# Performance work log

Hardware: AMD Instinct MI355X
Metric: run time of the kernel (lower is better)

## Reference

```python
import jax, jax.numpy as jnp
import numpy as np

B, L, E, H = 1024, 50, 256, 256
NEG = -1e9          # stands in for -inf masked_fill (exp(NEG) == 0 in fp32)
C_EXPL = 10.0       # tanh_exploration for the pointer head
N_GLIMPSES = 1


def setup_inputs() -> dict:
    key = jax.random.key(0)
    ks = jax.random.split(key, 20)
    s = 1.0 / np.sqrt(H).astype(np.float32)
    return {
        "decoder_input": jax.random.normal(ks[0], (B, E), jnp.float32),
        "embedded_inputs": jax.random.normal(ks[1], (L, B, E), jnp.float32),
        "h0": jax.random.normal(ks[2], (B, H), jnp.float32),
        "c0": jax.random.normal(ks[3], (B, H), jnp.float32),
        "context": jax.random.normal(ks[4], (L, B, H), jnp.float32),
        "init_mask": jnp.zeros((B, L), dtype=bool),
        "lstm_Wih": jax.random.normal(ks[5], (4 * H, E), jnp.float32) * s,
        "lstm_Whh": jax.random.normal(ks[6], (4 * H, H), jnp.float32) * s,
        "lstm_bih": jax.random.normal(ks[7], (4 * H,), jnp.float32) * s,
        "lstm_bhh": jax.random.normal(ks[8], (4 * H,), jnp.float32) * s,
        "gl_Wq": jax.random.normal(ks[9], (H, H), jnp.float32) * s,
        "gl_bq": jax.random.normal(ks[10], (H,), jnp.float32) * s,
        "gl_Wref": jax.random.normal(ks[11], (H, H), jnp.float32) * s,
        "gl_bref": jax.random.normal(ks[12], (H,), jnp.float32) * s,
        "gl_v": jax.random.uniform(ks[13], (H,), jnp.float32, -s, s),
        "pt_Wq": jax.random.normal(ks[14], (H, H), jnp.float32) * s,
        "pt_bq": jax.random.normal(ks[15], (H, H // H * H,)[:1] and (H,), jnp.float32) * s,
        "pt_Wref": jax.random.normal(ks[16], (H, H), jnp.float32) * s,
        "pt_bref": jax.random.normal(ks[17], (H,), jnp.float32) * s,
        "pt_v": jax.random.uniform(ks[18], (H,), jnp.float32, -s, s),
    }


def _attention(Wq, bq, Wref, bref, v, query, context, use_tanh):
    # context: [L,B,H], query: [B,H]
    e = jnp.einsum('lbh,oh->lbo', context, Wref) + bref      # conv1d(k=1) proj of ref
    q = query @ Wq.T + bq                                    # [B,H]
    u = jnp.einsum('lbh,h->bl', jnp.tanh(q[None, :, :] + e), v)
    if use_tanh:
        u = C_EXPL * jnp.tanh(u)
    return e, u


def _lstm_cell(x, h, c, Wih, Whh, bih, bhh):
    g = x @ Wih.T + bih + h @ Whh.T + bhh
    i, f, gg, o = jnp.split(g, 4, axis=1)   # torch LSTMCell gate order: i,f,g,o
    c2 = jax.nn.sigmoid(f) * c + jax.nn.sigmoid(i) * jnp.tanh(gg)
    h2 = jax.nn.sigmoid(o) * jnp.tanh(c2)
    return h2, c2


def reference(decoder_input, embedded_inputs, h0, c0, context, init_mask,
              lstm_Wih, lstm_Whh, lstm_bih, lstm_bhh,
              gl_Wq, gl_bq, gl_Wref, gl_bref, gl_v,
              pt_Wq, pt_bq, pt_Wref, pt_bref, pt_v):
    batch_idx = jnp.arange(B)

    def step(carry, t):
        h, c, mask, idxs, dec_in = carry
        # update_mask(mask, selected), skipped at step 0 (prev_idxs is None)
        safe = jnp.maximum(idxs, 0)
        m2 = mask.at[batch_idx, safe].set(True)
        m2 = m2.at[:, -1].set(jnp.where(m2.all(axis=1), False, m2[:, -1]))
        logit_mask = jnp.where(t == 0, mask, m2)
        # LSTM cell
        hy, cy = _lstm_cell(dec_in, h, c, lstm_Wih, lstm_Whh, lstm_bih, lstm_bhh)
        g_l = hy
        # glimpse attention(s) (mask_glimpses=True)
        for _ in range(N_GLIMPSES):
            e, gl = _attention(gl_Wq, gl_bq, gl_Wref, gl_bref, gl_v, g_l, context, False)
            gl = jnp.where(logit_mask, NEG, gl)
            g_l = jnp.einsum('lbh,bl->bh', e, jax.nn.softmax(gl, axis=1))
        # pointer attention (mask_logits=True)
        _, logits = _attention(pt_Wq, pt_bq, pt_Wref, pt_bref, pt_v, g_l, context, True)
        logits = jnp.where(logit_mask, NEG, logits)
        log_p = jax.nn.log_softmax(logits, axis=1)          # [B,L]
        new_idxs = jax.lax.stop_gradient(jnp.argmax(log_p, axis=1))  # greedy decode (detached)
        new_dec_in = embedded_inputs[new_idxs, batch_idx]   # gather next input [B,E]
        return (hy, cy, logit_mask, new_idxs, new_dec_in), (log_p, new_idxs)

    init = (h0, c0, init_mask, jnp.full((B,), -1, dtype=jnp.int32), decoder_input)
    _, (log_ps, sels) = jax.lax.scan(step, init, jnp.arange(L))
    # stack along time dim 1, as torch.stack(outputs, 1)
    return jnp.transpose(log_ps, (1, 0, 2)), jnp.transpose(sels, (1, 0))
```

## Files before the change

kernel.cpp:

```cpp
#include <hip/hip_runtime.h>
#include <math.h>

#define Bsz 1024
#define Lsz 50
#define Esz 256
#define Hsz 256
#define NEGV (-1e9f)

__global__ void init_kernel(const float* __restrict__ dec0,
                            float* __restrict__ dec,
                            int* __restrict__ mask)
{
    int i = blockIdx.x * 256 + threadIdx.x;
    dec[i] = dec0[i];
    if (i < Bsz * Lsz) mask[i] = 0;
}

__global__ void transpose_wq(const float* __restrict__ WqGl, const float* __restrict__ WqPt,
                             float* __restrict__ WqGlT, float* __restrict__ WqPtT)
{
    int k = blockIdx.x;
    int n = threadIdx.x;
    if (blockIdx.y == 0) WqGlT[k * 256 + n] = WqGl[n * 256 + k];
    else                 WqPtT[k * 256 + n] = WqPt[n * 256 + k];
}

__global__ __launch_bounds__(256) void eproj_kernel(const float* __restrict__ A,
                                                    const float* __restrict__ W,
                                                    const float* __restrict__ bias,
                                                    float* __restrict__ Eo)
{
    __shared__ __align__(16) float As[16][68];
    __shared__ __align__(16) float Bs[16][68];
    const int tid = threadIdx.x;
    const int tx = tid & 15, ty = tid >> 4;
    const int ml = tid >> 2;
    const int kb = (tid & 3) << 2;

    const int x = blockIdx.x;
    const int xcd = x & 7;
    const int j = x >> 3;
    const int mt = xcd * 100 + (j >> 2);
    const int nt = j & 3;
    const int m0 = mt * 64, n0 = nt * 64;

    const int K = Hsz;
    float acc[4][4] = {};
    for (int k0 = 0; k0 < K; k0 += 16) {
        float4 a4 = *(const float4*)(A + (size_t)(m0 + ml) * K + k0 + kb);
        float4 b4 = *(const float4*)(W + (size_t)(n0 + ml) * K + k0 + kb);
        As[kb+0][ml] = a4.x; As[kb+1][ml] = a4.y; As[kb+2][ml] = a4.z; As[kb+3][ml] = a4.w;
        Bs[kb+0][ml] = b4.x; Bs[kb+1][ml] = b4.y; Bs[kb+2][ml] = b4.z; Bs[kb+3][ml] = b4.w;
        __syncthreads();
#pragma unroll
        for (int kk = 0; kk < 16; kk++) {
            float4 av = *(const float4*)(&As[kk][ty << 2]);
            float4 bv = *(const float4*)(&Bs[kk][tx << 2]);
            float a_[4] = {av.x, av.y, av.z, av.w};
            float b_[4] = {bv.x, bv.y, bv.z, bv.w};
#pragma unroll
            for (int i = 0; i < 4; i++)
#pragma unroll
                for (int j2 = 0; j2 < 4; j2++) acc[i][j2] = fmaf(a_[i], b_[j2], acc[i][j2]);
        }
        __syncthreads();
    }
#pragma unroll
    for (int i = 0; i < 4; i++) {
        int m = m0 + (ty << 2) + i;
        int bb = m & (Bsz - 1);
        int ll = m >> 10;
#pragma unroll
        for (int j2 = 0; j2 < 4; j2++) {
            int n = n0 + (tx << 2) + j2;
            Eo[(size_t)bb * Lsz * Hsz + (size_t)ll * Hsz + n] = acc[i][j2] + bias[n];
        }
    }
}

__global__ __launch_bounds__(256) void lstm_fused(
    const float* __restrict__ dec, const float* __restrict__ hprev,
    const float* __restrict__ cin,
    const float* __restrict__ Wih, const float* __restrict__ Whh,
    const float* __restrict__ bih, const float* __restrict__ bhh,
    float* __restrict__ hout, float* __restrict__ cout)
{
    __shared__ __align__(16) float As[16][68];
    __shared__ __align__(16) float Bs[16][68];
    const int tid = threadIdx.x;
    const int tx = tid & 15, ty = tid >> 4;
    const int ml = tid >> 2;
    const int kb = (tid & 3) << 2;
    const int m0 = blockIdx.x * 64;
    const int hh0 = blockIdx.y * 16;
    const int wrow = ((ml >> 4) << 8) + hh0 + (ml & 15);
    const int pcol = ((ml & 15) << 2) + (ml >> 4);

    float4 a4 = *(const float4*)(dec + (size_t)(m0 + ml) * 256 + kb);
    float4 b4 = *(const float4*)(Wih + (size_t)wrow * 256 + kb);

    float acc[4][4] = {};
    for (int k0 = 0; k0 < 512; k0 += 16) {
        As[kb+0][ml] = a4.x; As[kb+1][ml] = a4.y; As[kb+2][ml] = a4.z; As[kb+3][ml] = a4.w;
        Bs[kb+0][pcol] = b4.x; Bs[kb+1][pcol] = b4.y; Bs[kb+2][pcol] = b4.z; Bs[kb+3][pcol] = b4.w;
        __syncthreads();
        int k1 = k0 + 16;
        if (k1 < 512) {
            const float* A = (k1 < 256) ? dec : hprev;
            const float* W = (k1 < 256) ? Wih : Whh;
            int kk0 = k1 & 255;
            a4 = *(const float4*)(A + (size_t)(m0 + ml) * 256 + kk0 + kb);
            b4 = *(const float4*)(W + (size_t)wrow * 256 + kk0 + kb);
        }
#pragma unroll
        for (int kk = 0; kk < 16; kk++) {
            float4 av = *(const float4*)(&As[kk][ty << 2]);
            float4 bv = *(const float4*)(&Bs[kk][tx << 2]);
            float a_[4] = {av.x, av.y, av.z, av.w};
            float b_[4] = {bv.x, bv.y, bv.z, bv.w};
#pragma unroll
            for (int i = 0; i < 4; i++)
#pragma unroll
                for (int j = 0; j < 4; j++) acc[i][j] = fmaf(a_[i], b_[j], acc[i][j]);
        }
        __syncthreads();
    }

    const int hh = hh0 + tx;
    const float bi0 = bih[hh]       + bhh[hh];
    const float bf  = bih[256 + hh] + bhh[256 + hh];
    const float bg  = bih[512 + hh] + bhh[512 + hh];
    const float bo  = bih[768 + hh] + bhh[768 + hh];
#pragma unroll
    for (int i = 0; i < 4; i++) {
        int m = m0 + (ty << 2) + i;
        float gi = acc[i][0] + bi0;
        float gf = acc[i][1] + bf;
        float gc = acc[i][2] + bg;
        float go = acc[i][3] + bo;
        float ii = 1.0f / (1.0f + expf(-gi));
        float ff = 1.0f / (1.0f + expf(-gf));
        float oo = 1.0f / (1.0f + expf(-go));
        float c2 = ff * cin[(size_t)m * 256 + hh] + ii * tanhf(gc);
        hout[(size_t)m * 256 + hh] = oo * tanhf(c2);
        cout[(size_t)m * 256 + hh] = c2;
    }
}

__global__ __launch_bounds__(256) void attn_row(
    const float* __restrict__ h,
    const float* __restrict__ WqGlT, const float* __restrict__ glbq,
    const float* __restrict__ e_gl, const float* __restrict__ glv,
    const float* __restrict__ WqPtT, const float* __restrict__ ptbq,
    const float* __restrict__ e_pt, const float* __restrict__ ptv,
    int* __restrict__ mask, float* __restrict__ out, int t,
    float* __restrict__ dec, const float* __restrict__ emb)
{
    __shared__ float h_s[256];
    __shared__ __align__(16) float q_s[256];
    __shared__ float g_s[256];
    __shared__ float u_s[64];
    __shared__ float p_s[64];
    __shared__ int sel_s;

    const int tid = threadIdx.x;
    const int lane = tid & 63, wave = tid >> 6;
    const int b = blockIdx.x;

    h_s[tid] = h[(size_t)b * 256 + tid];
    __syncthreads();

    float q = glbq[tid];
#pragma unroll 8
    for (int k = 0; k < 256; k++)
        q = fmaf(h_s[k], WqGlT[(size_t)k * 256 + tid], q);
    q_s[tid] = q;
    __syncthreads();

    const float* ebg = e_gl + (size_t)b * Lsz * 256;
    {
        const float4 q4 = ((const float4*)q_s)[lane];
        const float4 v4 = ((const float4*)glv)[lane];
#pragma unroll
        for (int lp = 0; lp < 13; lp++) {
            const int l = lp * 4 + wave;
            float x = 0.0f;
            if (l < Lsz) {
                float4 e4 = *(const float4*)(ebg + (size_t)l * 256 + (lane << 2));
                x  = v4.x * tanhf(q4.x + e4.x);
                x += v4.y * tanhf(q4.y + e4.y);
                x += v4.z * tanhf(q4.z + e4.z);
                x += v4.w * tanhf(q4.w + e4.w);
            }
#pragma unroll
            for (int o = 32; o > 0; o >>= 1) x += __shfl_xor(x, o, 64);
            if (lane == 0 && l < Lsz) u_s[l] = x;
        }
    }
    __syncthreads();

    if (wave == 0) {
        const int l = lane;
        const int ml = (l < Lsz) ? mask[b * Lsz + l] : 0;
        float logit = (l < Lsz) ? (ml ? NEGV : u_s[l]) : -1e30f;
        float m = logit;
#pragma unroll
        for (int o = 32; o > 0; o >>= 1) m = fmaxf(m, __shfl_xor(m, o, 64));
        float ex = (l < Lsz) ? expf(logit - m) : 0.0f;
        float den = ex;
#pragma unroll
        for (int o = 32; o > 0; o >>= 1) den += __shfl_xor(den, o, 64);
        if (l < Lsz) p_s[l] = ex / den;
    }
    __syncthreads();

    {
        float acc = 0.0f;
        const float* ebh = ebg + tid;
#pragma unroll
        for (int l = 0; l < Lsz; l++)
            acc = fmaf(p_s[l], ebh[(size_t)l * 256], acc);
        g_s[tid] = acc;
    }
    __syncthreads();

    float p = ptbq[tid];
#pragma unroll 8
    for (int k = 0; k < 256; k++)
        p = fmaf(g_s[k], WqPtT[(size_t)k * 256 + tid], p);
    q_s[tid] = p;
    __syncthreads();

    const float* ebp = e_pt + (size_t)b * Lsz * 256;
    {
        const float4 q4 = ((const float4*)q_s)[lane];
        const float4 v4 = ((const float4*)ptv)[lane];
#pragma unroll
        for (int lp = 0; lp < 13; lp++) {
            const int l = lp * 4 + wave;
            float x = 0.0f;
            if (l < Lsz) {
                float4 e4 = *(const float4*)(ebp + (size_t)l * 256 + (lane << 2));
                x  = v4.x * tanhf(q4.x + e4.x);
                x += v4.y * tanhf(q4.y + e4.y);
                x += v4.z * tanhf(q4.z + e4.z);
                x += v4.w * tanhf(q4.w + e4.w);
            }
#pragma unroll
            for (int o = 32; o > 0; o >>= 1) x += __shfl_xor(x, o, 64);
            if (lane == 0 && l < Lsz) u_s[l] = x;
        }
    }
    __syncthreads();

    if (wave == 0) {
        const int l = lane;
        const int ml = (l < Lsz) ? mask[b * Lsz + l] : 0;
        float logit;
        if (l < Lsz) {
            float u = u_s[l];
            logit = 10.0f * tanhf(u);
            if (ml) logit = NEGV;
        } else logit = -1e30f;

        float m = logit;
#pragma unroll
        for (int o = 32; o > 0; o >>= 1) m = fmaxf(m, __shfl_xor(m, o, 64));
        float ex = (l < Lsz) ? expf(logit - m) : 0.0f;
        float den = ex;
#pragma unroll
        for (int o = 32; o > 0; o >>= 1) den += __shfl_xor(den, o, 64);

        float av = logit; int ai = (l < Lsz) ? l : 63;
#pragma unroll
        for (int o = 32; o > 0; o >>= 1) {
            float ov = __shfl_xor(av, o, 64);
            int   oi = __shfl_xor(ai, o, 64);
            if (ov > av || (ov == av && oi < ai)) { av = ov; ai = oi; }
        }
        const float lse = m + logf(den);
        if (l < Lsz)
            out[(size_t)b * Lsz * Lsz + (size_t)t * Lsz + l] = logit - lse;
        if (l == 0) {
            out[(size_t)Bsz * Lsz * Lsz + (size_t)b * Lsz + t] = (float)ai;
            sel_s = ai;
        }
        int newm = ml | (l == ai);
        unsigned long long bal = __ballot(l >= Lsz ? 1 : newm);
        int all = (bal == 0xFFFFFFFFFFFFFFFFull);
        if (l < Lsz) mask[b * Lsz + l] = (all && l == Lsz - 1) ? 0 : newm;
    }
    __syncthreads();

    {
        const int s = sel_s;
        dec[(size_t)b * 256 + tid] = emb[(size_t)s * Bsz * 256 + (size_t)b * 256 + tid];
    }
}

extern "C" void kernel_launch(void* const* d_in, const int* in_sizes, int n_in,
                              void* d_out, int out_size, void* d_ws, size_t ws_size,
                              hipStream_t stream) {
    const float* decoder_input = (const float*)d_in[0];
    const float* emb           = (const float*)d_in[1];
    const float* h0            = (const float*)d_in[2];
    const float* c0            = (const float*)d_in[3];
    const float* context       = (const float*)d_in[4];
    const float* Wih    = (const float*)d_in[6];
    const float* Whh    = (const float*)d_in[7];
    const float* bih    = (const float*)d_in[8];
    const float* bhh    = (const float*)d_in[9];
    const float* glWq   = (const float*)d_in[10];
    const float* glbq   = (const float*)d_in[11];
    const float* glWref = (const float*)d_in[12];
    const float* glbref = (const float*)d_in[13];
    const float* glv    = (const float*)d_in[14];
    const float* ptWq   = (const float*)d_in[15];
    const float* ptbq   = (const float*)d_in[16];
    const float* ptWref = (const float*)d_in[17];
    const float* ptbref = (const float*)d_in[18];
    const float* ptv    = (const float*)d_in[19];

    float* out = (float*)d_out;

    float* ws    = (float*)d_ws;
    float* e_gl  = ws;
    float* e_pt  = e_gl + (size_t)Bsz * Lsz * Hsz;
    float* WqGlT = e_pt + (size_t)Bsz * Lsz * Hsz;
    float* WqPtT = WqGlT + (size_t)Hsz * Hsz;
    float* hb0   = WqPtT + (size_t)Hsz * Hsz;
    float* hb1   = hb0 + (size_t)Bsz * Hsz;
    float* cb0   = hb1 + (size_t)Bsz * Hsz;
    float* cb1   = cb0 + (size_t)Bsz * Hsz;
    float* dec   = cb1 + (size_t)Bsz * Hsz;
    int*   mask  = (int*)(dec + (size_t)Bsz * Esz);

    float* hbuf[2] = {hb0, hb1};
    float* cbuf[2] = {cb0, cb1};

    init_kernel<<<dim3(Bsz), dim3(256), 0, stream>>>(decoder_input, dec, mask);
    transpose_wq<<<dim3(256, 2), dim3(256), 0, stream>>>(glWq, ptWq, WqGlT, WqPtT);

    eproj_kernel<<<dim3(3200), dim3(256), 0, stream>>>(context, glWref, glbref, e_gl);
    eproj_kernel<<<dim3(3200), dim3(256), 0, stream>>>(context, ptWref, ptbref, e_pt);

    for (int t = 0; t < Lsz; t++) {
        const float* hin = (t == 0) ? h0 : hbuf[(t + 1) & 1];
        const float* cin = (t == 0) ? c0 : cbuf[(t + 1) & 1];
        float* hout = hbuf[t & 1];
        float* cout = cbuf[t & 1];

        lstm_fused<<<dim3(16, 16), dim3(256), 0, stream>>>(
            dec, hin, cin, Wih, Whh, bih, bhh, hout, cout);

        attn_row<<<dim3(Bsz), dim3(256), 0, stream>>>(
            hout, WqGlT, glbq, e_gl, glv, WqPtT, ptbq, e_pt, ptv,
            mask, out, t, dec, emb);
    }
}
```

Measured before the change: 4.383 ms.

## Pack Wq as float4, fuse both Wref projections, shrink LSTM tiles

Several changes land together. The query weights are repacked so each thread reads float4 (four k values) instead of scalar strided loads in the per-row attention query GEMVs. The two context projections are merged into one launch with register prefetch of the next k tile. The LSTM GEMM uses 32-row tiles, doubling the block count to 512 so more CUs are busy. These aim to cut load instructions in attn_row and to raise occupancy in the latency-bound per-step LSTM, at the cost of less register reuse per thread in the LSTM.

```diff
diff --git a/kernel.cpp b/kernel.cpp
--- a/kernel.cpp
+++ b/kernel.cpp
@@ -16,19 +16,20 @@
     if (i < Bsz * Lsz) mask[i] = 0;
 }
 
-__global__ void transpose_wq(const float* __restrict__ WqGl, const float* __restrict__ WqPt,
-                             float* __restrict__ WqGlT, float* __restrict__ WqPtT)
+__global__ void pack_wq(const float* __restrict__ WqGl, const float* __restrict__ WqPt,
+                        float* __restrict__ WqGlP, float* __restrict__ WqPtP)
 {
     int k = blockIdx.x;
     int n = threadIdx.x;
-    if (blockIdx.y == 0) WqGlT[k * 256 + n] = WqGl[n * 256 + k];
-    else                 WqPtT[k * 256 + n] = WqPt[n * 256 + k];
-}
-
-__global__ __launch_bounds__(256) void eproj_kernel(const float* __restrict__ A,
-                                                    const float* __restrict__ W,
-                                                    const float* __restrict__ bias,
-                                                    float* __restrict__ Eo)
+    const float* src = blockIdx.y ? WqPt : WqGl;
+    float*       dst = blockIdx.y ? WqPtP : WqGlP;
+    dst[((size_t)(k >> 2) * 256 + n) * 4 + (k & 3)] = src[(size_t)n * 256 + k];
+}
+
+__global__ __launch_bounds__(256) void eproj_kernel(
+    const float* __restrict__ A,
+    const float* __restrict__ Wgl, const float* __restrict__ bgl, float* __restrict__ Egl,
+    const float* __restrict__ Wpt, const float* __restrict__ bpt, float* __restrict__ Ept)
 {
     __shared__ __align__(16) float As[16][68];
     __shared__ __align__(16) float Bs[16][68];
@@ -40,18 +41,27 @@
     const int x = blockIdx.x;
     const int xcd = x & 7;
     const int j = x >> 3;
-    const int mt = xcd * 100 + (j >> 2);
+    const int mt = xcd * 100 + (j >> 3);
+    const int sel = (j >> 2) & 1;
     const int nt = j & 3;
+    const float* W    = sel ? Wpt : Wgl;
+    const float* bias = sel ? bpt : bgl;
+    float*       Eo   = sel ? Ept : Egl;
     const int m0 = mt * 64, n0 = nt * 64;
 
-    const int K = Hsz;
+    float4 a4 = *(const float4*)(A + (size_t)(m0 + ml) * 256 + kb);
+    float4 b4 = *(const float4*)(W + (size_t)(n0 + ml) * 256 + kb);
+
     float acc[4][4] = {};
-    for (int k0 = 0; k0 < K; k0 += 16) {
-        float4 a4 = *(const float4*)(A + (size_t)(m0 + ml) * K + k0 + kb);
-        float4 b4 = *(const float4*)(W + (size_t)(n0 + ml) * K + k0 + kb);
+    for (int k0 = 0; k0 < 256; k0 += 16) {
         As[kb+0][ml] = a4.x; As[kb+1][ml] = a4.y; As[kb+2][ml] = a4.z; As[kb+3][ml] = a4.w;
         Bs[kb+0][ml] = b4.x; Bs[kb+1][ml] = b4.y; Bs[kb+2][ml] = b4.z; Bs[kb+3][ml] = b4.w;
         __syncthreads();
+        int k1 = k0 + 16;
+        if (k1 < 256) {
+            a4 = *(const float4*)(A + (size_t)(m0 + ml) * 256 + k1 + kb);
+            b4 = *(const float4*)(W + (size_t)(n0 + ml) * 256 + k1 + kb);
+        }
 #pragma unroll
         for (int kk = 0; kk < 16; kk++) {
             float4 av = *(const float4*)(&As[kk][ty << 2]);
@@ -85,43 +95,48 @@
     const float* __restrict__ bih, const float* __restrict__ bhh,
     float* __restrict__ hout, float* __restrict__ cout)
 {
-    __shared__ __align__(16) float As[16][68];
+    __shared__ __align__(16) float As[16][36];
     __shared__ __align__(16) float Bs[16][68];
     const int tid = threadIdx.x;
     const int tx = tid & 15, ty = tid >> 4;
-    const int ml = tid >> 2;
-    const int kb = (tid & 3) << 2;
-    const int m0 = blockIdx.x * 64;
+    const int mlA = tid >> 3;
+    const int kbA = (tid & 7) << 1;
+    const int mlB = tid >> 2;
+    const int kbB = (tid & 3) << 2;
+    const int m0 = blockIdx.x * 32;
     const int hh0 = blockIdx.y * 16;
-    const int wrow = ((ml >> 4) << 8) + hh0 + (ml & 15);
-    const int pcol = ((ml & 15) << 2) + (ml >> 4);
-
-    float4 a4 = *(const float4*)(dec + (size_t)(m0 + ml) * 256 + kb);
-    float4 b4 = *(const float4*)(Wih + (size_t)wrow * 256 + kb);
-
-    float acc[4][4] = {};
+    const int wrow = ((mlB >> 4) << 8) + hh0 + (mlB & 15);
+    const int pcol = ((mlB & 15) << 2) + (mlB >> 4);
+
+    float2 a2 = *(const float2*)(dec + (size_t)(m0 + mlA) * 256 + kbA);
+    float4 b4 = *(const float4*)(Wih + (size_t)wrow * 256 + kbB);
+
+    float acc[2][4] = {};
     for (int k0 = 0; k0 < 512; k0 += 16) {
-        As[kb+0][ml] = a4.x; As[kb+1][ml] = a4.y; As[kb+2][ml] = a4.z; As[kb+3][ml] = a4.w;
-        Bs[kb+0][pcol] = b4.x; Bs[kb+1][pcol] = b4.y; Bs[kb+2][pcol] = b4.z; Bs[kb+3][pcol] = b4.w;
+        As[kbA+0][mlA] = a2.x; As[kbA+1][mlA] = a2.y;
+        Bs[kbB+0][pcol] = b4.x; Bs[kbB+1][pcol] = b4.y;
+        Bs[kbB+2][pcol] = b4.z; Bs[kbB+3][pcol] = b4.w;
         __syncthreads();
         int k1 = k0 + 16;
         if (k1 < 512) {
-            const float* A = (k1 < 256) ? dec : hprev;
-            const float* W = (k1 < 256) ? Wih : Whh;
+            const float* Ap = (k1 < 256) ? dec : hprev;
+            const float* Wp = (k1 < 256) ? Wih : Whh;
             int kk0 = k1 & 255;
-            a4 = *(const float4*)(A + (size_t)(m0 + ml) * 256 + kk0 + kb);
-            b4 = *(const float4*)(W + (size_t)wrow * 256 + kk0 + kb);
+            a2 = *(const float2*)(Ap + (size_t)(m0 + mlA) * 256 + kk0 + kbA);
+            b4 = *(const float4*)(Wp + (size_t)wrow * 256 + kk0 + kbB);
         }
 #pragma unroll
         for (int kk = 0; kk < 16; kk++) {
-            float4 av = *(const float4*)(&As[kk][ty << 2]);
+            float2 av = *(const float2*)(&As[kk][ty << 1]);
             float4 bv = *(const float4*)(&Bs[kk][tx << 2]);
-            float a_[4] = {av.x, av.y, av.z, av.w};
-            float b_[4] = {bv.x, bv.y, bv.z, bv.w};
-#pragma unroll
-            for (int i = 0; i < 4; i++)
-#pragma unroll
-                for (int j = 0; j < 4; j++) acc[i][j] = fmaf(a_[i], b_[j], acc[i][j]);
+            acc[0][0] = fmaf(av.x, bv.x, acc[0][0]);
+            acc[0][1] = fmaf(av.x, bv.y, acc[0][1]);
+            acc[0][2] = fmaf(av.x, bv.z, acc[0][2]);
+            acc[0][3] = fmaf(av.x, bv.w, acc[0][3]);
+            acc[1][0] = fmaf(av.y, bv.x, acc[1][0]);
+            acc[1][1] = fmaf(av.y, bv.y, acc[1][1]);
+            acc[1][2] = fmaf(av.y, bv.z, acc[1][2]);
+            acc[1][3] = fmaf(av.y, bv.w, acc[1][3]);
         }
         __syncthreads();
     }
@@ -132,8 +147,8 @@
     const float bg  = bih[512 + hh] + bhh[512 + hh];
     const float bo  = bih[768 + hh] + bhh[768 + hh];
 #pragma unroll
-    for (int i = 0; i < 4; i++) {
-        int m = m0 + (ty << 2) + i;
+    for (int i = 0; i < 2; i++) {
+        int m = m0 + (ty << 1) + i;
         float gi = acc[i][0] + bi0;
         float gf = acc[i][1] + bf;
         float gc = acc[i][2] + bg;
@@ -149,16 +164,16 @@
 
 __global__ __launch_bounds__(256) void attn_row(
     const float* __restrict__ h,
-    const float* __restrict__ WqGlT, const float* __restrict__ glbq,
+    const float* __restrict__ WqGlP, const float* __restrict__ glbq,
     const float* __restrict__ e_gl, const float* __restrict__ glv,
-    const float* __restrict__ WqPtT, const float* __restrict__ ptbq,
+    const float* __restrict__ WqPtP, const float* __restrict__ ptbq,
     const float* __restrict__ e_pt, const float* __restrict__ ptv,
     int* __restrict__ mask, float* __restrict__ out, int t,
     float* __restrict__ dec, const float* __restrict__ emb)
 {
-    __shared__ float h_s[256];
+    __shared__ __align__(16) float h_s[256];
     __shared__ __align__(16) float q_s[256];
-    __shared__ float g_s[256];
+    __shared__ __align__(16) float g_s[256];
     __shared__ float u_s[64];
     __shared__ float p_s[64];
     __shared__ int sel_s;
@@ -170,11 +185,20 @@
     h_s[tid] = h[(size_t)b * 256 + tid];
     __syncthreads();
 
-    float q = glbq[tid];
+    {
+        float q = glbq[tid];
+        const float4* Wp = (const float4*)WqGlP;
 #pragma unroll 8
-    for (int k = 0; k < 256; k++)
-        q = fmaf(h_s[k], WqGlT[(size_t)k * 256 + tid], q);
-    q_s[tid] = q;
+        for (int k4 = 0; k4 < 64; k4++) {
+            float4 w  = Wp[(size_t)k4 * 256 + tid];
+            float4 hv = ((const float4*)h_s)[k4];
+            q = fmaf(hv.x, w.x, q);
+            q = fmaf(hv.y, w.y, q);
+            q = fmaf(hv.z, w.z, q);
+            q = fmaf(hv.w, w.w, q);
+        }
+        q_s[tid] = q;
+    }
     __syncthreads();
 
     const float* ebg = e_gl + (size_t)b * Lsz * 256;
@@ -224,11 +248,20 @@
     }
     __syncthreads();
 
-    float p = ptbq[tid];
+    {
+        float p = ptbq[tid];
+        const float4* Wp = (const float4*)WqPtP;
 #pragma unroll 8
-    for (int k = 0; k < 256; k++)
-        p = fmaf(g_s[k], WqPtT[(size_t)k * 256 + tid], p);
-    q_s[tid] = p;
+        for (int k4 = 0; k4 < 64; k4++) {
+            float4 w  = Wp[(size_t)k4 * 256 + tid];
+            float4 gv = ((const float4*)g_s)[k4];
+            p = fmaf(gv.x, w.x, p);
+            p = fmaf(gv.y, w.y, p);
+            p = fmaf(gv.z, w.z, p);
+            p = fmaf(gv.w, w.w, p);
+        }
+        q_s[tid] = p;
+    }
     __syncthreads();
 
     const float* ebp = e_pt + (size_t)b * Lsz * 256;
@@ -326,9 +359,9 @@
     float* ws    = (float*)d_ws;
     float* e_gl  = ws;
     float* e_pt  = e_gl + (size_t)Bsz * Lsz * Hsz;
-    float* WqGlT = e_pt + (size_t)Bsz * Lsz * Hsz;
-    float* WqPtT = WqGlT + (size_t)Hsz * Hsz;
-    float* hb0   = WqPtT + (size_t)Hsz * Hsz;
+    float* WqGlP = e_pt + (size_t)Bsz * Lsz * Hsz;
+    float* WqPtP = WqGlP + (size_t)Hsz * Hsz;
+    float* hb0   = WqPtP + (size_t)Hsz * Hsz;
     float* hb1   = hb0 + (size_t)Bsz * Hsz;
     float* cb0   = hb1 + (size_t)Bsz * Hsz;
     float* cb1   = cb0 + (size_t)Bsz * Hsz;
@@ -339,10 +372,10 @@
     float* cbuf[2] = {cb0, cb1};
 
     init_kernel<<<dim3(Bsz), dim3(256), 0, stream>>>(decoder_input, dec, mask);
-    transpose_wq<<<dim3(256, 2), dim3(256), 0, stream>>>(glWq, ptWq, WqGlT, WqPtT);
-
-    eproj_kernel<<<dim3(3200), dim3(256), 0, stream>>>(context, glWref, glbref, e_gl);
-    eproj_kernel<<<dim3(3200), dim3(256), 0, stream>>>(context, ptWref, ptbref, e_pt);
+    pack_wq<<<dim3(256, 2), dim3(256), 0, stream>>>(glWq, ptWq, WqGlP, WqPtP);
+
+    eproj_kernel<<<dim3(6400), dim3(256), 0, stream>>>(
+        context, glWref, glbref, e_gl, ptWref, ptbref, e_pt);
 
     for (int t = 0; t < Lsz; t++) {
         const float* hin = (t == 0) ? h0 : hbuf[(t + 1) & 1];
@@ -350,11 +383,11 @@
         float* hout = hbuf[t & 1];
         float* cout = cbuf[t & 1];
 
-        lstm_fused<<<dim3(16, 16), dim3(256), 0, stream>>>(
+        lstm_fused<<<dim3(32, 16), dim3(256), 0, stream>>>(
             dec, hin, cin, Wih, Whh, bih, bhh, hout, cout);
 
         attn_row<<<dim3(Bsz), dim3(256), 0, stream>>>(
-            hout, WqGlT, glbq, e_gl, glv, WqPtT, ptbq, e_pt, ptv,
+            hout, WqGlP, glbq, e_gl, glv, WqPtP, ptbq, e_pt, ptv,
             mask, out, t, dec, emb);
     }
 }
```

Result: faster. 4.145 ms (-5.4%).
